# Optimization experiments

Measured on AMD Instinct MI355X. Metric: run time of the kernel, lower is better.

## Reference

```python
import jax, jax.numpy as jnp
import numpy as np

SQ, B, NP, HN = 2048, 2, 16, 64  # [seq, batch, heads, head_dim]

def setup_inputs() -> dict:
    key = jax.random.key(0)
    kq, kk, kv = jax.random.split(key, 3)
    return {
        "query": jax.random.normal(kq, (SQ, B, NP, HN), dtype=jnp.float32),
        "key":   jax.random.normal(kk, (SQ, B, NP, HN), dtype=jnp.float32),
        "value": jax.random.normal(kv, (SQ, B, NP, HN), dtype=jnp.float32),
    }

def reference(query, key, value):
    sq, b, nheads, hn = query.shape
    # NOTE: original module computes norm_factor=sqrt(hn) but never applies it;
    # scores are UNscaled QK^T, replicated faithfully here.
    scores = jnp.einsum('sbnh,tbnh->bnst', query, key)          # [b, np, sq, sk]
    probs = jax.nn.softmax(scores, axis=-1)                      # mask=None -> plain softmax
    # dropout is deterministic (train=False default) -> identity
    context = jnp.einsum('bnst,tbnh->sbnh', probs, value)        # [sq, b, np, hn]
    return context.reshape(sq, b, nheads * hn).astype(jnp.float32)
```

## Files before the change

### kernel.cpp

```cpp
#include <hip/hip_runtime.h>
#include <math.h>
#include <stdint.h>

#define SQ 2048
#define NBH 32
#define HN 64
#define BQ 128
#define BK2 128
#define NP2 (SQ/BK2)
#define TOK 2048
#define HSTRIDE (SQ*HN)

typedef _Float16 half2v __attribute__((ext_vector_type(2)));
typedef _Float16 half4v __attribute__((ext_vector_type(4)));
typedef _Float16 half8v __attribute__((ext_vector_type(8)));
typedef float f32x16 __attribute__((ext_vector_type(16)));

__device__ __forceinline__ void async16(const void* g, void* l) {
  __builtin_amdgcn_global_load_lds(
      (const __attribute__((address_space(1))) void*)g,
      (__attribute__((address_space(3))) void*)l, 16, 0, 0);
}

__device__ __forceinline__ float fexp2(float x) {
#if __has_builtin(__builtin_amdgcn_exp2f)
  return __builtin_amdgcn_exp2f(x);
#else
  return exp2f(x);
#endif
}

__device__ __forceinline__ float xmax32(float x) {
#if __has_builtin(__builtin_amdgcn_permlane32_swap)
  auto r = __builtin_amdgcn_permlane32_swap(__float_as_int(x), __float_as_int(x),
                                            false, false);
  return fmaxf(__int_as_float(r[0]), __int_as_float(r[1]));
#else
  return fmaxf(x, __shfl_xor(x, 32, 64));
#endif
}
__device__ __forceinline__ float xadd32(float x) {
#if __has_builtin(__builtin_amdgcn_permlane32_swap)
  auto r = __builtin_amdgcn_permlane32_swap(__float_as_int(x), __float_as_int(x),
                                            false, false);
  return __int_as_float(r[0]) + __int_as_float(r[1]);
#else
  return x + __shfl_xor(x, 32, 64);
#endif
}

__global__ __launch_bounds__(256) void prep_kv(const float* __restrict__ K,
                                               const float* __restrict__ V,
                                               _Float16* __restrict__ Kh,
                                               _Float16* __restrict__ Vt) {
  __shared__ _Float16 vs[HN * 64];
  const int t = threadIdx.x;
  const int head = blockIdx.y;
  {
    const int key = blockIdx.x * 64 + (t >> 2);
    const int c0 = (t & 3) * 2;
    const float* src = K + (size_t)key * TOK + head * HN + c0 * 8;
    float4 a = *(const float4*)src;
    float4 b = *(const float4*)(src + 4);
    float4 c = *(const float4*)(src + 8);
    float4 d = *(const float4*)(src + 12);
    half8v h0, h1;
    h0[0]=(_Float16)a.x; h0[1]=(_Float16)a.y; h0[2]=(_Float16)a.z; h0[3]=(_Float16)a.w;
    h0[4]=(_Float16)b.x; h0[5]=(_Float16)b.y; h0[6]=(_Float16)b.z; h0[7]=(_Float16)b.w;
    h1[0]=(_Float16)c.x; h1[1]=(_Float16)c.y; h1[2]=(_Float16)c.z; h1[3]=(_Float16)c.w;
    h1[4]=(_Float16)d.x; h1[5]=(_Float16)d.y; h1[6]=(_Float16)d.z; h1[7]=(_Float16)d.w;
    _Float16* row = Kh + (size_t)head * HSTRIDE + (size_t)key * 64;
    *(half8v*)&row[((c0    ) ^ (key & 7)) * 8] = h0;
    *(half8v*)&row[((c0 + 1) ^ (key & 7)) * 8] = h1;
  }
  {
    const int kt = blockIdx.x * 64;
    const int kl = (t >> 3) * 2;
    const int db = (t & 7) * 8;
    const float* src = V + (size_t)(kt + kl) * TOK + head * HN + db;
    float4 a0 = *(const float4*)src;
    float4 a1 = *(const float4*)(src + 4);
    float4 b0 = *(const float4*)(src + TOK);
    float4 b1 = *(const float4*)(src + TOK + 4);
    const float av[8] = {a0.x,a0.y,a0.z,a0.w,a1.x,a1.y,a1.z,a1.w};
    const float bv[8] = {b0.x,b0.y,b0.z,b0.w,b1.x,b1.y,b1.z,b1.w};
    const int u = kl >> 2;
    #pragma unroll
    for (int j = 0; j < 8; ++j) {
      const int dim = db + j;
      const int pos = u ^ (dim & 15);
      half2v h; h[0] = (_Float16)av[j]; h[1] = (_Float16)bv[j];
      *(half2v*)&vs[dim * 64 + pos * 4 + (kl & 3)] = h;
    }
    __syncthreads();
    const int dim = t >> 2;
    const int q = (t & 3) ^ (dim & 3);
    const _Float16* srow = &vs[dim * 64 + q * 16];
    _Float16* drow = Vt + (size_t)head * HSTRIDE + (size_t)dim * SQ + kt + q * 16;
    *(half8v*)&drow[0] = *(const half8v*)&srow[0];
    *(half8v*)&drow[8] = *(const half8v*)&srow[8];
  }
}

__global__ __launch_bounds__(512, 4)
void fattn_mfma(const float* __restrict__ Q, const _Float16* __restrict__ Kh,
                const _Float16* __restrict__ Vt, float* __restrict__ O) {
  __shared__ __align__(16) _Float16 smem[4 * 8192];
  _Float16* kbf = smem;
  _Float16* vtf = smem + 16384;

  const int t = threadIdx.x;
  const int lane = t & 63;
  const int w = t >> 6;
  const int qw = w & 3;
  const int g = w >> 2;
  const int h2 = lane >> 5;
  const int l31 = lane & 31;
  const int q0 = blockIdx.x * BQ + qw * 32;
  const int head = blockIdx.y;
  const _Float16* Kp = Kh + (size_t)head * HSTRIDE;
  const _Float16* Vp = Vt + (size_t)head * HSTRIDE;
  const int tb = g * 4096;

  half8v qf[4];
  {
    const float* qp = Q + (size_t)(q0 + l31) * TOK + head * HN + 8 * h2;
    const float s = 1.44269504088896f;
    #pragma unroll
    for (int ks = 0; ks < 4; ++ks) {
      float4 a = *(const float4*)(qp + 16 * ks);
      float4 b = *(const float4*)(qp + 16 * ks + 4);
      half8v f;
      f[0] = (_Float16)(s*a.x); f[1] = (_Float16)(s*a.y); f[2] = (_Float16)(s*a.z); f[3] = (_Float16)(s*a.w);
      f[4] = (_Float16)(s*b.x); f[5] = (_Float16)(s*b.y); f[6] = (_Float16)(s*b.z); f[7] = (_Float16)(s*b.w);
      qf[ks] = f;
    }
  }

  f32x16 acc0, acc1;
  #pragma unroll
  for (int r = 0; r < 16; ++r) { acc0[r] = 0.f; acc1[r] = 0.f; }
  float m_i = -INFINITY, l_i = 0.f;

  auto stage = [&](int p) {
    const int buf = p & 1;
    const size_t kt = (size_t)p * BK2;
    #pragma unroll
    for (int i = 0; i < 2; ++i) {
      const int off = w * 512 + i * 4096;
      async16(Kp + kt * 64 + off + lane * 8, kbf + buf * 8192 + off);
    }
    #pragma unroll
    for (int tl = 0; tl < 2; ++tl) {
      const int off = w * 512;
      const int eo = off + lane * 8;
      const int dim = eo >> 6, inner = eo & 63;
      async16(Vp + (size_t)dim * SQ + kt + tl * 64 + inner,
              vtf + buf * 8192 + tl * 4096 + off);
    }
  };

  stage(0);
  for (int p = 0; p < NP2; ++p) {
    __syncthreads();
    if (p + 1 < NP2) stage(p + 1);
    const int cur = p & 1;
    const _Float16* kb = kbf + cur * 8192 + tb;
    const _Float16* vb = vtf + cur * 8192 + tb;

    f32x16 c0, c1;
    #pragma unroll
    for (int r = 0; r < 16; ++r) { c0[r] = 0.f; c1[r] = 0.f; }
    __builtin_amdgcn_s_setprio(1);
    #pragma unroll
    for (int ks = 0; ks < 4; ++ks) {
      const int pos = ((h2 + 2 * ks) ^ (l31 & 7)) * 8;
      half8v a0v = *(const half8v*)&kb[l31 * 64 + pos];
      half8v a1v = *(const half8v*)&kb[(l31 + 32) * 64 + pos];
      c0 = __builtin_amdgcn_mfma_f32_32x32x16_f16(a0v, qf[ks], c0, 0, 0, 0);
      c1 = __builtin_amdgcn_mfma_f32_32x32x16_f16(a1v, qf[ks], c1, 0, 0, 0);
    }
    __builtin_amdgcn_s_setprio(0);

    float mx0 = fmaxf(c0[0], c1[0]);
    float mx1 = fmaxf(c0[1], c1[1]);
    float mx2 = fmaxf(c0[2], c1[2]);
    float mx3 = fmaxf(c0[3], c1[3]);
    #pragma unroll
    for (int r = 4; r < 16; r += 4) {
      mx0 = fmaxf(mx0, fmaxf(c0[r],     c1[r]));
      mx1 = fmaxf(mx1, fmaxf(c0[r + 1], c1[r + 1]));
      mx2 = fmaxf(mx2, fmaxf(c0[r + 2], c1[r + 2]));
      mx3 = fmaxf(mx3, fmaxf(c0[r + 3], c1[r + 3]));
    }
    float mx = xmax32(fmaxf(fmaxf(mx0, mx1), fmaxf(mx2, mx3)));
    if (!__all(mx <= m_i + 8.f)) {
      const float mnew = fmaxf(m_i, mx);
      const float alpha = fexp2(m_i - mnew);
      l_i *= alpha;
      m_i = mnew;
      #pragma unroll
      for (int r = 0; r < 16; ++r) { acc0[r] *= alpha; acc1[r] *= alpha; }
    }
    float rs0 = 0.f, rs1 = 0.f;
    #pragma unroll
    for (int r = 0; r < 16; ++r) {
      float p0 = fexp2(c0[r] - m_i);
      float p1 = fexp2(c1[r] - m_i);
      c0[r] = p0; c1[r] = p1;
      rs0 += p0; rs1 += p1;
    }
    l_i += xadd32(rs0 + rs1);

    __builtin_amdgcn_s_setprio(1);
    #pragma unroll
    for (int ks = 0; ks < 4; ++ks) {
      const int rb = 8 * (ks & 1);
      const f32x16& s = (ks < 2) ? c0 : c1;
      union { half8v v8; half2v v2[4]; } pu;
      #pragma unroll
      for (int tt = 0; tt < 4; ++tt) {
        auto pk = __builtin_amdgcn_cvt_pkrtz(s[rb + 2 * tt], s[rb + 2 * tt + 1]);
        pu.v2[tt] = *(half2v*)&pk;
      }
      #pragma unroll
      for (int mbd = 0; mbd < 2; ++mbd) {
        const int dim = l31 + 32 * mbd;
        const int sw = dim & 15;
        union { half8v v8; half4v v4[2]; } au;
        au.v4[0] = *(const half4v*)&vtf[cur * 8192 + tb + dim * 64 + ((4 * ks + h2)     ^ sw) * 4];
        au.v4[1] = *(const half4v*)&vtf[cur * 8192 + tb + dim * 64 + ((4 * ks + 2 + h2) ^ sw) * 4];
        if (mbd == 0)
          acc0 = __builtin_amdgcn_mfma_f32_32x32x16_f16(au.v8, pu.v8, acc0, 0, 0, 0);
        else
          acc1 = __builtin_amdgcn_mfma_f32_32x32x16_f16(au.v8, pu.v8, acc1, 0, 0, 0);
      }
    }
    __builtin_amdgcn_s_setprio(0);
    (void)vb;
  }

  __syncthreads();
  float* fb = (float*)smem;
  const int slot = qw * 64 + lane;
  if (g == 1) {
    #pragma unroll
    for (int r = 0; r < 16; ++r) {
      fb[slot * 32 + r]      = acc0[r];
      fb[slot * 32 + 16 + r] = acc1[r];
    }
    fb[8192 + slot] = m_i;
    fb[8448 + slot] = l_i;
  }
  __syncthreads();
  if (g == 0) {
    const float m2 = fb[8192 + slot];
    const float l2 = fb[8448 + slot];
    const float ms = fmaxf(m_i, m2);
    const float a0 = fexp2(m_i - ms);
    const float a1 = fexp2(m2 - ms);
    const float invl = 1.f / (l_i * a0 + l2 * a1);
    float* orow = O + (size_t)(q0 + l31) * TOK + head * HN;
    #pragma unroll
    for (int r = 0; r < 16; ++r) {
      const int d = (r & 3) + 8 * (r >> 2) + 4 * h2;
      orow[d]      = (acc0[r] * a0 + fb[slot * 32 + r]      * a1) * invl;
      orow[d + 32] = (acc1[r] * a0 + fb[slot * 32 + 16 + r] * a1) * invl;
    }
  }
}

extern "C" void kernel_launch(void* const* d_in, const int* in_sizes, int n_in,
                              void* d_out, int out_size, void* d_ws, size_t ws_size,
                              hipStream_t stream) {
  const float* Q = (const float*)d_in[0];
  const float* K = (const float*)d_in[1];
  const float* V = (const float*)d_in[2];
  float* O = (float*)d_out;
  _Float16* Kh = (_Float16*)d_ws;
  _Float16* Vh = Kh + (size_t)NBH * HSTRIDE;
  prep_kv<<<dim3(SQ / 64, NBH), 256, 0, stream>>>(K, V, Kh, Vh);
  fattn_mfma<<<dim3(SQ / BQ, NBH), 512, 0, stream>>>(Q, Kh, Vh, O);
}
```

Measured before the change: 143.9 us.

## Remap block-to-head order for cache locality and unroll double-buffer phases

Block indices in both the prep and attention kernels are remapped so that consecutively scheduled blocks cover 8 heads interleaved across query/key chunks, aiming for better L2/MALL reuse of each head's K/V data across CUs. The main loop is split into a lambda called twice per iteration with constant buffer indices, so LDS offsets become compile-time constants. The row-max reduction is restructured into 3-input max trees, which may map to v_max3. Code size grows, and the change in block scheduling may help or hurt locality.

```diff
diff --git a/kernel.cpp b/kernel.cpp
--- a/kernel.cpp
+++ b/kernel.cpp
@@ -55,9 +55,11 @@
                                                _Float16* __restrict__ Vt) {
   __shared__ _Float16 vs[HN * 64];
   const int t = threadIdx.x;
-  const int head = blockIdx.y;
+  const int pflat = blockIdx.y * 32 + blockIdx.x;
+  const int head = (pflat & 7) + 8 * (pflat >> 8);
+  const int ck = (pflat >> 3) & 31;
   {
-    const int key = blockIdx.x * 64 + (t >> 2);
+    const int key = ck * 64 + (t >> 2);
     const int c0 = (t & 3) * 2;
     const float* src = K + (size_t)key * TOK + head * HN + c0 * 8;
     float4 a = *(const float4*)src;
@@ -74,7 +76,7 @@
     *(half8v*)&row[((c0 + 1) ^ (key & 7)) * 8] = h1;
   }
   {
-    const int kt = blockIdx.x * 64;
+    const int kt = ck * 64;
     const int kl = (t >> 3) * 2;
     const int db = (t & 7) * 8;
     const float* src = V + (size_t)(kt + kl) * TOK + head * HN + db;
@@ -116,8 +118,10 @@
   const int g = w >> 2;
   const int h2 = lane >> 5;
   const int l31 = lane & 31;
-  const int q0 = blockIdx.x * BQ + qw * 32;
-  const int head = blockIdx.y;
+  const int pflat = blockIdx.y * 16 + blockIdx.x;
+  const int head = (pflat & 7) + 8 * (pflat >> 7);
+  const int qc = (pflat >> 3) & 15;
+  const int q0 = qc * BQ + qw * 32;
   const _Float16* Kp = Kh + (size_t)head * HSTRIDE;
   const _Float16* Vp = Vt + (size_t)head * HSTRIDE;
   const int tb = g * 4096;
@@ -160,11 +164,9 @@
     }
   };
 
-  stage(0);
-  for (int p = 0; p < NP2; ++p) {
+  auto phase = [&](int p, int cur) {
     __syncthreads();
     if (p + 1 < NP2) stage(p + 1);
-    const int cur = p & 1;
     const _Float16* kb = kbf + cur * 8192 + tb;
     const _Float16* vb = vtf + cur * 8192 + tb;
 
@@ -182,18 +184,16 @@
     }
     __builtin_amdgcn_s_setprio(0);
 
-    float mx0 = fmaxf(c0[0], c1[0]);
-    float mx1 = fmaxf(c0[1], c1[1]);
-    float mx2 = fmaxf(c0[2], c1[2]);
-    float mx3 = fmaxf(c0[3], c1[3]);
-    #pragma unroll
-    for (int r = 4; r < 16; r += 4) {
-      mx0 = fmaxf(mx0, fmaxf(c0[r],     c1[r]));
-      mx1 = fmaxf(mx1, fmaxf(c0[r + 1], c1[r + 1]));
-      mx2 = fmaxf(mx2, fmaxf(c0[r + 2], c1[r + 2]));
-      mx3 = fmaxf(mx3, fmaxf(c0[r + 3], c1[r + 3]));
-    }
-    float mx = xmax32(fmaxf(fmaxf(mx0, mx1), fmaxf(mx2, mx3)));
+    float tv[16];
+    #pragma unroll
+    for (int r = 0; r < 16; ++r) tv[r] = fmaxf(c0[r], c1[r]);
+    float ma = fmaxf(fmaxf(tv[0], tv[1]), tv[2]);
+    float mb = fmaxf(fmaxf(tv[3], tv[4]), tv[5]);
+    float mc = fmaxf(fmaxf(tv[6], tv[7]), tv[8]);
+    float md = fmaxf(fmaxf(tv[9], tv[10]), tv[11]);
+    ma = fmaxf(fmaxf(ma, tv[12]), tv[13]);
+    mb = fmaxf(fmaxf(mb, tv[14]), tv[15]);
+    float mx = xmax32(fmaxf(fmaxf(ma, mb), fmaxf(mc, md)));
     if (!__all(mx <= m_i + 8.f)) {
       const float mnew = fmaxf(m_i, mx);
       const float alpha = fexp2(m_i - mnew);
@@ -228,8 +228,8 @@
         const int dim = l31 + 32 * mbd;
         const int sw = dim & 15;
         union { half8v v8; half4v v4[2]; } au;
-        au.v4[0] = *(const half4v*)&vtf[cur * 8192 + tb + dim * 64 + ((4 * ks + h2)     ^ sw) * 4];
-        au.v4[1] = *(const half4v*)&vtf[cur * 8192 + tb + dim * 64 + ((4 * ks + 2 + h2) ^ sw) * 4];
+        au.v4[0] = *(const half4v*)&vb[dim * 64 + ((4 * ks + h2)     ^ sw) * 4];
+        au.v4[1] = *(const half4v*)&vb[dim * 64 + ((4 * ks + 2 + h2) ^ sw) * 4];
         if (mbd == 0)
           acc0 = __builtin_amdgcn_mfma_f32_32x32x16_f16(au.v8, pu.v8, acc0, 0, 0, 0);
         else
@@ -237,7 +237,13 @@
       }
     }
     __builtin_amdgcn_s_setprio(0);
-    (void)vb;
+  };
+
+  stage(0);
+  #pragma unroll 1
+  for (int p = 0; p < NP2; p += 2) {
+    phase(p, 0);
+    phase(p + 1, 1);
   }
 
   __syncthreads();
```

After: 141.2 us. Within noise of the previous version (-1.9%).
